# Optimization experiments

Measured on AMD Instinct MI355X. Metric: run time of the kernel, lower is better.

Reference implementation:

```python
import jax, jax.numpy as jnp
import numpy as np

N, E, H, C = 50000, 800000, 4, 32   # nodes, edges, heads, per-head channels
EMB = 64                              # embedding_dim
VOCAB = 1000                          # input_dim (label vocab)


def _gat_layer(x, src, dst, W, a_src, a_dst, b):
    """PyG GATConv (concat heads, negative_slope=0.2, self-loops already in src/dst)."""
    n = x.shape[0]
    h = (x @ W).reshape(n, H, -1)                 # [N,H,C]
    al_s = (h * a_src).sum(-1)                    # [N,H]
    al_d = (h * a_dst).sum(-1)                    # [N,H]
    e = jax.nn.leaky_relu(al_s[src] + al_d[dst], 0.2)   # [E',H]
    m = jax.ops.segment_max(e, dst, num_segments=n)     # segment softmax (stable)
    p = jnp.exp(e - m[dst])
    s = jax.ops.segment_sum(p, dst, num_segments=n)
    alpha = p / (s[dst] + 1e-16)                  # [E',H]
    out = jax.ops.segment_sum(h[src] * alpha[..., None], dst, num_segments=n)
    return out.reshape(n, -1) + b                 # [N,H*C]


def setup_inputs() -> dict:
    key = jax.random.key(0)
    ks = jax.random.split(key, 16)
    def w(k, shape):
        return jax.random.normal(k, shape, jnp.float32) * 0.1
    return dict(
        label=jax.random.randint(ks[0], (N,), 0, VOCAB),
        edge_index=jax.random.randint(ks[1], (2, E), 0, N),
        weight=jax.random.uniform(ks[2], (E,), jnp.float32),
        request_quantity=jax.random.uniform(ks[3], (N,), jnp.float32),
        emb_table=w(ks[4], (VOCAB, EMB)),
        req_W=w(ks[5], (1, EMB)),
        req_b=jnp.zeros((EMB,), jnp.float32),
        W0=w(ks[6], (2 * EMB, H * C)), a_src0=w(ks[7], (H, C)), a_dst0=w(ks[8], (H, C)), b0=jnp.zeros((H * C,), jnp.float32),
        W1=w(ks[9], (H * C, H * C)), a_src1=w(ks[10], (H, C)), a_dst1=w(ks[11], (H, C)), b1=jnp.zeros((H * C,), jnp.float32),
        W2=w(ks[12], (H * C, H * C)), a_src2=w(ks[13], (H, C)), a_dst2=w(ks[14], (H, C)), b2=jnp.zeros((H * C,), jnp.float32),
    )


def reference(label, edge_index, weight, request_quantity, emb_table, req_W, req_b,
              W0, a_src0, a_dst0, b0, W1, a_src1, a_dst1, b1, W2, a_src2, a_dst2, b2):
    del weight  # GATConv(edge_dim=None): edge weights are not used in attention
    x_emb = emb_table[label]                                  # [N,EMB]
    rq = request_quantity
    rq = (rq - rq.mean()) / (rq.std(ddof=1) + 1e-6)           # torch std uses ddof=1
    req = rq[:, None] @ req_W + req_b                         # [N,EMB]
    x = jnp.concatenate([x_emb, req], axis=-1)                # [N,2*EMB]
    # PyG GATConv adds self-loops by default
    loops = jnp.arange(N)
    src = jnp.concatenate([edge_index[0], loops])
    dst = jnp.concatenate([edge_index[1], loops])
    gelu = lambda t: jax.nn.gelu(t, approximate=False)        # torch nn.GELU is exact
    x = gelu(_gat_layer(x, src, dst, W0, a_src0, a_dst0, b0))
    x = gelu(_gat_layer(x, src, dst, W1, a_src1, a_dst1, b1))
    x = gelu(_gat_layer(x, src, dst, W2, a_src2, a_dst2, b2))
    return x
```

## Files before the change

kernel.cpp:

```cpp
#include <hip/hip_runtime.h>
#include <hip/hip_fp16.h>
#include <math.h>

#define NN 50000
#define NE 800000
#define HC 128
#define NHEAD 4
#define EMB 64
#define STATS_BLOCKS 64
#define NB 196
#define HIST_BLOCKS 196
#define WPREP_BLOCKS 192
#define WT_ROW 136

typedef _Float16 f16x8 __attribute__((ext_vector_type(8)));
typedef float f32x4 __attribute__((ext_vector_type(4)));

__device__ __forceinline__ float lrelu(float x) { return x > 0.0f ? x : 0.2f * x; }
__device__ __forceinline__ float gelu_f(float x) {
    return 0.5f * x * (1.0f + erff(x * 0.70710678118654752440f));
}
__device__ __forceinline__ float sel4(float4 v, int h) {
    float r = v.x;
    r = (h == 1) ? v.y : r;
    r = (h == 2) ? v.z : r;
    r = (h == 3) ? v.w : r;
    return r;
}
__device__ __forceinline__ f16x8 cvt8(float4 a, float4 b) {
    f16x8 v;
    v[0] = (_Float16)a.x; v[1] = (_Float16)a.y; v[2] = (_Float16)a.z; v[3] = (_Float16)a.w;
    v[4] = (_Float16)b.x; v[5] = (_Float16)b.y; v[6] = (_Float16)b.z; v[7] = (_Float16)b.w;
    return v;
}

__global__ void prep_kernel(const float* __restrict__ rq, float* __restrict__ stats,
                            const int* __restrict__ dst, int* __restrict__ bucketCnt,
                            const float* __restrict__ W0, const float* __restrict__ W1,
                            const float* __restrict__ W2, _Float16* __restrict__ wt) {
    __shared__ float ls[4], ls2[4];
    __shared__ int cnt[NB];
    if (blockIdx.x < STATS_BLOCKS) {
        int i = blockIdx.x * 256 + threadIdx.x;
        float s = 0.f, s2 = 0.f;
        for (; i < NN; i += STATS_BLOCKS * 256) {
            float v = rq[i];
            s += v; s2 += v * v;
        }
        #pragma unroll
        for (int off = 32; off > 0; off >>= 1) {
            s  += __shfl_down(s, off);
            s2 += __shfl_down(s2, off);
        }
        int lane = threadIdx.x & 63, wid = threadIdx.x >> 6;
        if (lane == 0) { ls[wid] = s; ls2[wid] = s2; }
        __syncthreads();
        if (threadIdx.x == 0) {
            atomicAdd(&stats[0], ls[0] + ls[1] + ls[2] + ls[3]);
            atomicAdd(&stats[1], ls2[0] + ls2[1] + ls2[2] + ls2[3]);
        }
    } else if (blockIdx.x < STATS_BLOCKS + HIST_BLOCKS) {
        int bb = blockIdx.x - STATS_BLOCKS;
        for (int i = threadIdx.x; i < NB; i += 256) cnt[i] = 0;
        __syncthreads();
        int base = bb * 4096;
        #pragma unroll
        for (int it = 0; it < 16; it++) {
            int i = base + it * 256 + threadIdx.x;
            if (i < NE) atomicAdd(&cnt[dst[i] >> 8], 1);
        }
        __syncthreads();
        for (int i = threadIdx.x; i < NB; i += 256)
            if (cnt[i]) atomicAdd(&bucketCnt[i], cnt[i]);
    } else {
        int bb = blockIdx.x - STATS_BLOCKS - HIST_BLOCKS;
        int l = bb >> 6, blk = bb & 63;
        const float* W = (l == 0) ? W0 : (l == 1) ? W1 : W2;
        int idx = blk * 256 + threadIdx.x;
        int n = idx >> 7, k = idx & 127;
        wt[(size_t)l * 128 * WT_ROW + n * WT_ROW + k] = (_Float16)W[k * 128 + n];
    }
}

__device__ __forceinline__ void scan_buckets(const int* __restrict__ bucketCnt,
                                             int* sIncl ) {
    int t = threadIdx.x;
    int v = (t < NB) ? bucketCnt[t] : 0;
    sIncl[t] = v;
    __syncthreads();
    #pragma unroll
    for (int off = 1; off < 256; off <<= 1) {
        int add = (t >= off) ? sIncl[t - off] : 0;
        __syncthreads();
        sIncl[t] += add;
        __syncthreads();
    }
}

__global__ void binA_kernel(const int* __restrict__ src, const int* __restrict__ dst,
                            const int* __restrict__ bucketCnt, int* __restrict__ gcur,
                            int2* __restrict__ edge_tmp) {
    __shared__ int sIncl[256];
    __shared__ int sBaseE[256];
    __shared__ int cnt[NB];
    __shared__ int cur[NB];
    int t = threadIdx.x;
    scan_buckets(bucketCnt, sIncl);
    {
        int v = (t < NB) ? bucketCnt[t] : 0;
        sBaseE[t] = sIncl[t] - v;
    }
    for (int i = t; i < NB; i += 256) cnt[i] = 0;
    __syncthreads();
    int base = blockIdx.x * 4096;
    int d[16], s[16];
    #pragma unroll
    for (int it = 0; it < 16; it++) {
        int i = base + it * 256 + t;
        bool ok = i < NE;
        d[it] = ok ? dst[i] : -1;
        s[it] = ok ? src[i] : 0;
        if (ok) atomicAdd(&cnt[d[it] >> 8], 1);
    }
    __syncthreads();
    for (int i = t; i < NB; i += 256)
        cur[i] = cnt[i] ? (sBaseE[i] + atomicAdd(&gcur[i], cnt[i])) : 0;
    __syncthreads();
    #pragma unroll
    for (int it = 0; it < 16; it++) {
        if (d[it] >= 0) {
            int b = d[it] >> 8;
            int pos = atomicAdd(&cur[b], 1);
            edge_tmp[pos] = make_int2(s[it], d[it] & 255);
        }
    }
}

__global__ void binB_kernel(const int2* __restrict__ edge_tmp, const int* __restrict__ bucketCnt,
                            int* __restrict__ row_start, int* __restrict__ src_sorted) {
    __shared__ int sIncl[256];
    __shared__ int ldeg[256];
    __shared__ int lexcl[256];
    __shared__ int lcur[256];
    __shared__ int s_base, s_end;
    int b = blockIdx.x, t = threadIdx.x;
    scan_buckets(bucketCnt, sIncl);
    if (t == 0) {
        s_end = sIncl[b];
        s_base = sIncl[b] - bucketCnt[b];
    }
    ldeg[t] = 0;
    __syncthreads();
    int base = s_base, endb = s_end;
    for (int i = base + t; i < endb; i += 256)
        atomicAdd(&ldeg[edge_tmp[i].y], 1);
    __syncthreads();
    int v = ldeg[t];
    lexcl[t] = v;
    __syncthreads();
    #pragma unroll
    for (int off = 1; off < 256; off <<= 1) {
        int add = (t >= off) ? lexcl[t - off] : 0;
        __syncthreads();
        lexcl[t] += add;
        __syncthreads();
    }
    int excl = lexcl[t] - v;
    int node = b * 256 + t;
    if (node <= NN) row_start[node] = base + excl;
    lcur[t] = excl;
    __syncthreads();
    for (int i = base + t; i < endb; i += 256) {
        int2 e = edge_tmp[i];
        int pos = atomicAdd(&lcur[e.y], 1);
        src_sorted[base + pos] = e.x;
    }
}

template <int L0>
__launch_bounds__(256)
__global__ void gemm_al_kernel(const __half* __restrict__ xh, const _Float16* __restrict__ wt,
                               const float* __restrict__ a_src, const float* __restrict__ a_dst,
                               __half* __restrict__ h, float* __restrict__ als,
                               float* __restrict__ ald,
                               const int* __restrict__ label, const float* __restrict__ rq,
                               const float* __restrict__ emb, const float* __restrict__ reqW,
                               const float* __restrict__ reqb, const float* __restrict__ stats) {
    extern __shared__ char smem[];
    _Float16* sWt = (_Float16*)smem;
    _Float16* sX  = sWt + 128 * WT_ROW;
    int t = threadIdx.x;
    int w = t >> 6, l = t & 63;
    int col = l & 15, quad = l >> 4;
    int row0 = blockIdx.x * 64;

    {
        const f16x8* g = (const f16x8*)wt;
        f16x8* s = (f16x8*)sWt;
        #pragma unroll
        for (int i = 0; i < 9; i++) {
            int idx = t + 256 * i;
            if (idx < 128 * WT_ROW / 8) s[idx] = g[idx];
        }
    }
    if (L0) {
        float sum = stats[0], sumsq = stats[1];
        float mean = sum / (float)NN;
        float var = (sumsq - sum * sum / (float)NN) / (float)(NN - 1);
        float inv = 1.0f / (sqrtf(var) + 1e-6f);
        #pragma unroll
        for (int i = 0; i < 4; i++) {
            int idx = t + 256 * i;
            int r = idx >> 4;
            int q = idx & 15;
            int rr = row0 + r;
            f16x8 v;
            #pragma unroll
            for (int j = 0; j < 8; j++) v[j] = (_Float16)0.f;
            if (rr < NN) {
                if (q < 8) {
                    const float4* er = (const float4*)(emb + (size_t)label[rr] * EMB);
                    v = cvt8(er[q * 2], er[q * 2 + 1]);
                } else {
                    int j4 = (q - 8) * 2;
                    float4 w0 = ((const float4*)reqW)[j4],     b0 = ((const float4*)reqb)[j4];
                    float4 w1 = ((const float4*)reqW)[j4 + 1], b1 = ((const float4*)reqb)[j4 + 1];
                    float r2 = (rq[rr] - mean) * inv;
                    v = cvt8(make_float4(r2 * w0.x + b0.x, r2 * w0.y + b0.y,
                                         r2 * w0.z + b0.z, r2 * w0.w + b0.w),
                             make_float4(r2 * w1.x + b1.x, r2 * w1.y + b1.y,
                                         r2 * w1.z + b1.z, r2 * w1.w + b1.w));
                }
            }
            *(f16x8*)&sX[r * WT_ROW + q * 8] = v;
        }
    }
    __syncthreads();

    f16x8 afr[4];
    if (L0) {
        #pragma unroll
        for (int ks = 0; ks < 4; ks++)
            afr[ks] = *(const f16x8*)&sX[(w * 16 + col) * WT_ROW + ks * 32 + quad * 8];
    } else {
        int rr = row0 + w * 16 + col;
        const __half* xp = xh + (size_t)rr * 128;
        #pragma unroll
        for (int ks = 0; ks < 4; ks++)
            afr[ks] = *(const f16x8*)(xp + ks * 32 + quad * 8);
    }

    f32x4 zero = {0.f, 0.f, 0.f, 0.f};
    f32x4 acc[8];
    #pragma unroll
    for (int nt = 0; nt < 8; nt++) acc[nt] = zero;
    #pragma unroll
    for (int nt = 0; nt < 8; nt++) {
        #pragma unroll
        for (int ks = 0; ks < 4; ks++) {
            f16x8 bfr = *(const f16x8*)&sWt[(nt * 16 + col) * WT_ROW + ks * 32 + quad * 8];
            acc[nt] = __builtin_amdgcn_mfma_f32_16x16x32_f16(afr[ks], bfr, acc[nt], 0, 0, 0);
        }
    }
    __syncthreads();

    _Float16* sOut = sWt;
    #pragma unroll
    for (int nt = 0; nt < 8; nt++)
        #pragma unroll
        for (int r = 0; r < 4; r++)
            sOut[(w * 16 + quad * 4 + r) * WT_ROW + nt * 16 + col] = (_Float16)acc[nt][r];
    __builtin_amdgcn_wave_barrier();
    #pragma unroll
    for (int i = 0; i < 4; i++) {
        int u = l + 64 * i;
        int r = u >> 4, off = (u & 15) * 8;
        int rr = row0 + w * 16 + r;
        f16x8 v = *(const f16x8*)&sOut[(w * 16 + r) * WT_ROW + off];
        if (rr < NN) *(f16x8*)(h + (size_t)rr * 128 + off) = v;
    }

    float as[8], ad[8];
    #pragma unroll
    for (int nt = 0; nt < 8; nt++) {
        as[nt] = a_src[nt * 16 + col];
        ad[nt] = a_dst[nt * 16 + col];
    }
    #pragma unroll
    for (int r = 0; r < 4; r++) {
        float ps[4], pd[4];
        #pragma unroll
        for (int hd = 0; hd < 4; hd++) {
            ps[hd] = acc[2 * hd][r] * as[2 * hd] + acc[2 * hd + 1][r] * as[2 * hd + 1];
            pd[hd] = acc[2 * hd][r] * ad[2 * hd] + acc[2 * hd + 1][r] * ad[2 * hd + 1];
            ps[hd] += __shfl_xor(ps[hd], 1); pd[hd] += __shfl_xor(pd[hd], 1);
            ps[hd] += __shfl_xor(ps[hd], 2); pd[hd] += __shfl_xor(pd[hd], 2);
            ps[hd] += __shfl_xor(ps[hd], 4); pd[hd] += __shfl_xor(pd[hd], 4);
            ps[hd] += __shfl_xor(ps[hd], 8); pd[hd] += __shfl_xor(pd[hd], 8);
        }
        int rr = row0 + w * 16 + quad * 4 + r;
        if (col == 0 && rr < NN) {
            *(float4*)(als + (size_t)rr * 4) = make_float4(ps[0], ps[1], ps[2], ps[3]);
            *(float4*)(ald + (size_t)rr * 4) = make_float4(pd[0], pd[1], pd[2], pd[3]);
        }
    }
}

template <int FINAL>
__launch_bounds__(256)
__global__ void agg_kernel(const __half* __restrict__ h, const float* __restrict__ als_,
                           const float* __restrict__ ald_, const int* __restrict__ row_start,
                           const int* __restrict__ src_sorted, const float* __restrict__ bias,
                           float* __restrict__ outf, __half* __restrict__ outh) {
    __shared__ int2 lds_sp[4][4][66];
    int wid  = threadIdx.x >> 6;
    int lane = threadIdx.x & 63;
    int g    = lane >> 4;
    int cg   = lane & 15;
    int c0   = cg * 8;
    int head = cg >> 2;

    int nb = blockIdx.x * 16 + wid * 4;
    if (nb >= NN) return;
    int node = nb + g;

    int rs = row_start[node];
    int re = row_start[node + 1];
    int start = __shfl(rs, 0);
    int end   = __shfl(re, 48);
    int b1 = __shfl(rs, 16), b2 = __shfl(rs, 32), b3 = __shfl(rs, 48);

    float4 adv = *(const float4*)(ald_ + (size_t)node * 4);
    float4 avs = *(const float4*)(als_ + (size_t)node * 4);

    float p_self = __expf(lrelu(sel4(avs, head) + sel4(adv, head)));
    float s_sum = p_self;
    float acc[8];
    {
        f16x8 hv = *(const f16x8*)(h + (size_t)node * 128 + c0);
        #pragma unroll
        for (int j = 0; j < 8; j++) acc[j] = (float)hv[j] * p_self;
    }

    for (int base = start; base < end; base += 64) {
        int j = base + lane;
        bool v = j < end;
        int my = v ? src_sorted[j] : 0;
        float4 av = *(const float4*)(als_ + (size_t)my * 4);
        int o = (j >= b1) + (j >= b2) + (j >= b3);
        int ol = o << 4;
        float dx = __shfl(adv.x, ol), dy = __shfl(adv.y, ol);
        float dz = __shfl(adv.z, ol), dw = __shfl(adv.w, ol);
        lds_sp[wid][0][lane] = make_int2(my, __float_as_int(__expf(lrelu(av.x + dx))));
        lds_sp[wid][1][lane] = make_int2(my, __float_as_int(__expf(lrelu(av.y + dy))));
        lds_sp[wid][2][lane] = make_int2(my, __float_as_int(__expf(lrelu(av.z + dz))));
        lds_sp[wid][3][lane] = make_int2(my, __float_as_int(__expf(lrelu(av.w + dw))));
        __builtin_amdgcn_wave_barrier();

        int lo  = rs > base ? rs : base;
        int hiw = base + 64;
        int hi  = re < hiw ? re : hiw;
        for (int k = lo; k < hi; k += 4) {
            int sidx[4]; float p[4];
            #pragma unroll
            for (int i = 0; i < 4; i++) {
                int e = k + i;
                bool val = e < hi;
                int ec = (val ? e : hi - 1) - base;
                int2 sp = lds_sp[wid][head][ec];
                sidx[i] = sp.x;
                p[i] = val ? __int_as_float(sp.y) : 0.f;
            }
            f16x8 raw[4];
            #pragma unroll
            for (int i = 0; i < 4; i++)
                raw[i] = *(const f16x8*)(h + (size_t)sidx[i] * 128 + c0);
            #pragma unroll
            for (int i = 0; i < 4; i++) {
                s_sum += p[i];
                #pragma unroll
                for (int jj = 0; jj < 8; jj++)
                    acc[jj] += (float)raw[i][jj] * p[i];
            }
        }
        __builtin_amdgcn_wave_barrier();
    }

    float invs = 1.0f / (s_sum + 1e-16f);
    float4 bv0 = *(const float4*)(bias + c0);
    float4 bv1 = *(const float4*)(bias + c0 + 4);
    float ob[8] = {bv0.x, bv0.y, bv0.z, bv0.w, bv1.x, bv1.y, bv1.z, bv1.w};
    float o8[8];
    #pragma unroll
    for (int jj = 0; jj < 8; jj++) o8[jj] = gelu_f(acc[jj] * invs + ob[jj]);
    if (FINAL) {
        float* op = outf + (size_t)node * 128 + c0;
        *(float4*)op       = make_float4(o8[0], o8[1], o8[2], o8[3]);
        *(float4*)(op + 4) = make_float4(o8[4], o8[5], o8[6], o8[7]);
    } else {
        f16x8 hv;
        #pragma unroll
        for (int jj = 0; jj < 8; jj++) hv[jj] = (_Float16)o8[jj];
        *(f16x8*)(outh + (size_t)node * 128 + c0) = hv;
    }
}

extern "C" void kernel_launch(void* const* d_in, const int* in_sizes, int n_in,
                              void* d_out, int out_size, void* d_ws, size_t ws_size,
                              hipStream_t stream) {
    const int*   label = (const int*)d_in[0];
    const int*   eidx  = (const int*)d_in[1];
    const float* rq    = (const float*)d_in[3];
    const float* emb   = (const float*)d_in[4];
    const float* reqW  = (const float*)d_in[5];
    const float* reqb  = (const float*)d_in[6];
    const float* W[3]    = {(const float*)d_in[7],  (const float*)d_in[11], (const float*)d_in[15]};
    const float* asrc[3] = {(const float*)d_in[8],  (const float*)d_in[12], (const float*)d_in[16]};
    const float* adst[3] = {(const float*)d_in[9],  (const float*)d_in[13], (const float*)d_in[17]};
    const float* bias[3] = {(const float*)d_in[10], (const float*)d_in[14], (const float*)d_in[18]};

    const int* e_src = eidx;
    const int* e_dst = eidx + NE;

    char* ws = (char*)d_ws;
    size_t off = 0;
    auto A = [&](size_t n) { size_t o = off; off += (n + 255) & ~(size_t)255; return o; };
    size_t o_bcnt  = A(256 * 4);
    size_t o_gcur  = A(256 * 4);
    size_t o_stats = A(8);
    size_t zero_bytes = off;
    size_t o_row   = A((size_t)(NN + 1) * 4);
    size_t o_etmp  = A((size_t)NE * 8);
    size_t o_srcS  = A((size_t)NE * 4);
    size_t o_wt    = A((size_t)3 * 128 * WT_ROW * 2);
    size_t o_x     = A((size_t)NN * 128 * 2);
    size_t o_h     = A((size_t)NN * 128 * 2);
    size_t o_als   = A((size_t)NN * 4 * 4);
    size_t o_ald   = A((size_t)NN * 4 * 4);
    (void)ws_size; (void)n_in; (void)in_sizes; (void)out_size;

    int*      bcnt  = (int*)(ws + o_bcnt);
    int*      gcur  = (int*)(ws + o_gcur);
    float*    stats = (float*)(ws + o_stats);
    int*      rowst = (int*)(ws + o_row);
    int2*     etmp  = (int2*)(ws + o_etmp);
    int*      srcS  = (int*)(ws + o_srcS);
    _Float16* wt    = (_Float16*)(ws + o_wt);
    __half*   xh    = (__half*)(ws + o_x);
    __half*   h     = (__half*)(ws + o_h);
    float*    als   = (float*)(ws + o_als);
    float*    ald   = (float*)(ws + o_ald);

    (void)hipMemsetAsync(ws, 0, zero_bytes, stream);

    prep_kernel<<<STATS_BLOCKS + HIST_BLOCKS + WPREP_BLOCKS, 256, 0, stream>>>(
        rq, stats, e_dst, bcnt, W[0], W[1], W[2], wt);
    binA_kernel<<<HIST_BLOCKS, 256, 0, stream>>>(e_src, e_dst, bcnt, gcur, etmp);
    binB_kernel<<<NB, 256, 0, stream>>>(etmp, bcnt, rowst, srcS);

    const int gemm_blocks = (NN + 63) / 64;
    const int agg_blocks = (NN + 15) / 16;
    const int smem_l0 = (128 + 64) * WT_ROW * 2;
    const int smem_ln = 128 * WT_ROW * 2;
    for (int l = 0; l < 3; l++) {
        const _Float16* wtl = wt + (size_t)l * 128 * WT_ROW;
        if (l == 0)
            gemm_al_kernel<1><<<gemm_blocks, 256, smem_l0, stream>>>(
                xh, wtl, asrc[l], adst[l], h, als, ald, label, rq, emb, reqW, reqb, stats);
        else
            gemm_al_kernel<0><<<gemm_blocks, 256, smem_ln, stream>>>(
                xh, wtl, asrc[l], adst[l], h, als, ald, label, rq, emb, reqW, reqb, stats);
        if (l == 2)
            agg_kernel<1><<<agg_blocks, 256, 0, stream>>>(h, als, ald, rowst, srcS, bias[l],
                                                          (float*)d_out, nullptr);
        else
            agg_kernel<0><<<agg_blocks, 256, 0, stream>>>(h, als, ald, rowst, srcS, bias[l],
                                                          nullptr, xh);
    }
}
```

Before: 296.7 us.

## Widen edge staging chunk to 128 and unroll gather loop by 16

The aggregation kernel now stages 128 edges per wave iteration instead of 64, loading two source indices and attention logits per lane. It replaces the cross-lane shuffle of destination logits with direct float4 loads from global memory. The inner gather loop is unrolled to 16 outstanding f16x8 loads instead of 4, to raise memory-level parallelism on the irregular row gathers. In exchange it uses more registers (16 raw vectors) and twice the LDS, which may reduce occupancy, and it wastes more work on padded edges for low-degree nodes.

```diff
diff --git a/kernel.cpp b/kernel.cpp
--- a/kernel.cpp
+++ b/kernel.cpp
@@ -312,7 +312,7 @@
                            const float* __restrict__ ald_, const int* __restrict__ row_start,
                            const int* __restrict__ src_sorted, const float* __restrict__ bias,
                            float* __restrict__ outf, __half* __restrict__ outh) {
-    __shared__ int2 lds_sp[4][4][66];
+    __shared__ int2 lds_sp[4][4][130];
     int wid  = threadIdx.x >> 6;
     int lane = threadIdx.x & 63;
     int g    = lane >> 4;
@@ -342,41 +342,48 @@
         for (int j = 0; j < 8; j++) acc[j] = (float)hv[j] * p_self;
     }
 
-    for (int base = start; base < end; base += 64) {
-        int j = base + lane;
-        bool v = j < end;
-        int my = v ? src_sorted[j] : 0;
-        float4 av = *(const float4*)(als_ + (size_t)my * 4);
-        int o = (j >= b1) + (j >= b2) + (j >= b3);
-        int ol = o << 4;
-        float dx = __shfl(adv.x, ol), dy = __shfl(adv.y, ol);
-        float dz = __shfl(adv.z, ol), dw = __shfl(adv.w, ol);
-        lds_sp[wid][0][lane] = make_int2(my, __float_as_int(__expf(lrelu(av.x + dx))));
-        lds_sp[wid][1][lane] = make_int2(my, __float_as_int(__expf(lrelu(av.y + dy))));
-        lds_sp[wid][2][lane] = make_int2(my, __float_as_int(__expf(lrelu(av.z + dz))));
-        lds_sp[wid][3][lane] = make_int2(my, __float_as_int(__expf(lrelu(av.w + dw))));
+    for (int base = start; base < end; base += 128) {
+        int j0 = base + lane, j1 = base + 64 + lane;
+        bool v0 = j0 < end, v1 = j1 < end;
+        int my0 = v0 ? src_sorted[j0] : 0;
+        int my1 = v1 ? src_sorted[j1] : 0;
+        float4 av0 = *(const float4*)(als_ + (size_t)my0 * 4);
+        float4 av1 = *(const float4*)(als_ + (size_t)my1 * 4);
+        int o0 = (j0 >= b1) + (j0 >= b2) + (j0 >= b3);
+        int o1 = (j1 >= b1) + (j1 >= b2) + (j1 >= b3);
+        float4 d0 = *(const float4*)(ald_ + (size_t)(nb + (o0 > 3 ? 3 : o0)) * 4);
+        float4 d1 = *(const float4*)(ald_ + (size_t)(nb + (o1 > 3 ? 3 : o1)) * 4);
+        lds_sp[wid][0][lane] = make_int2(my0, __float_as_int(__expf(lrelu(av0.x + d0.x))));
+        lds_sp[wid][1][lane] = make_int2(my0, __float_as_int(__expf(lrelu(av0.y + d0.y))));
+        lds_sp[wid][2][lane] = make_int2(my0, __float_as_int(__expf(lrelu(av0.z + d0.z))));
+        lds_sp[wid][3][lane] = make_int2(my0, __float_as_int(__expf(lrelu(av0.w + d0.w))));
+        lds_sp[wid][0][64 + lane] = make_int2(my1, __float_as_int(__expf(lrelu(av1.x + d1.x))));
+        lds_sp[wid][1][64 + lane] = make_int2(my1, __float_as_int(__expf(lrelu(av1.y + d1.y))));
+        lds_sp[wid][2][64 + lane] = make_int2(my1, __float_as_int(__expf(lrelu(av1.z + d1.z))));
+        lds_sp[wid][3][64 + lane] = make_int2(my1, __float_as_int(__expf(lrelu(av1.w + d1.w))));
         __builtin_amdgcn_wave_barrier();
 
         int lo  = rs > base ? rs : base;
-        int hiw = base + 64;
+        int hiw = base + 128;
         int hi  = re < hiw ? re : hiw;
-        for (int k = lo; k < hi; k += 4) {
-            int sidx[4]; float p[4];
+        for (int k = lo; k < hi; k += 16) {
+            float p[16];
+            const __half* ap[16];
             #pragma unroll
-            for (int i = 0; i < 4; i++) {
+            for (int i = 0; i < 16; i++) {
                 int e = k + i;
                 bool val = e < hi;
                 int ec = (val ? e : hi - 1) - base;
                 int2 sp = lds_sp[wid][head][ec];
-                sidx[i] = sp.x;
                 p[i] = val ? __int_as_float(sp.y) : 0.f;
+                ap[i] = h + (size_t)sp.x * 128 + c0;
             }
-            f16x8 raw[4];
+            f16x8 raw[16];
             #pragma unroll
-            for (int i = 0; i < 4; i++)
-                raw[i] = *(const f16x8*)(h + (size_t)sidx[i] * 128 + c0);
+            for (int i = 0; i < 16; i++)
+                raw[i] = *(const f16x8*)ap[i];
             #pragma unroll
-            for (int i = 0; i < 4; i++) {
+            for (int i = 0; i < 16; i++) {
                 s_sum += p[i];
                 #pragma unroll
                 for (int jj = 0; jj < 8; jj++)
```

Result: no change. 293.6 us (-1.0%).
